# Kernel optimization log

Measured on AMD Instinct MI355X. Metric: run time of the kernel, lower is better.

Reference implementation:

```python
import jax, jax.numpy as jnp
from jax import lax
import numpy as np

# ---- constants mirroring args ----
T = 8192          # signal length
NUM_CH = 64       # eeg channels
LSTM_SIZE = 256
NUM_CLS = 40
NUM_PROP = 1024   # candidate proposals before NMS
NUM_PROP_AFTER = 256
PROP_LEN = 128    # extracted window length
IOU_THRESH = 0.5


def setup_inputs() -> dict:
    key = jax.random.key(0)
    ks = jax.random.split(key, 12)
    data = jax.random.normal(ks[0], (T, NUM_CH), dtype=jnp.float32)
    # proposals: (start, end, score), 1-D temporal intervals
    starts = jax.random.uniform(ks[1], (NUM_PROP,), minval=0.0, maxval=float(T - PROP_LEN))
    lens = jax.random.uniform(ks[2], (NUM_PROP,), minval=32.0, maxval=float(PROP_LEN))
    scores = jax.random.uniform(ks[3], (NUM_PROP,))
    proposals = jnp.stack([starts, starts + lens, scores], axis=-1).astype(jnp.float32)

    H, C = LSTM_SIZE, NUM_CH
    s_ih = 1.0 / np.sqrt(C)
    s_hh = 1.0 / np.sqrt(H)
    W_ih = jax.random.uniform(ks[4], (4 * H, C), minval=-s_ih, maxval=s_ih)
    W_hh = jax.random.uniform(ks[5], (4 * H, H), minval=-s_hh, maxval=s_hh)
    b_ih = jax.random.uniform(ks[6], (4 * H,), minval=-s_hh, maxval=s_hh)
    b_hh = jax.random.uniform(ks[7], (4 * H,), minval=-s_hh, maxval=s_hh)
    s_h = 1.0 / np.sqrt(H)
    W_cls = jax.random.uniform(ks[8], (NUM_CLS, H), minval=-s_h, maxval=s_h)
    b_cls = jax.random.uniform(ks[9], (NUM_CLS,), minval=-s_h, maxval=s_h)
    W_bbox = jax.random.uniform(ks[10], (2 * NUM_CLS, H), minval=-s_h, maxval=s_h)
    b_bbox = jax.random.uniform(ks[11], (2 * NUM_CLS,), minval=-s_h, maxval=s_h)
    return {"data": data, "proposals": proposals, "W_ih": W_ih, "W_hh": W_hh,
            "b_ih": b_ih, "b_hh": b_hh, "W_cls": W_cls, "b_cls": b_cls,
            "W_bbox": W_bbox, "b_bbox": b_bbox}


def _nms_1d(starts, ends, scores, iou_thresh):
    """Greedy 1-D interval NMS. Returns indices (into original order) of the
    first NUM_PROP_AFTER surviving proposals, in descending-score order."""
    order = jnp.argsort(-scores)
    s, e = starts[order], ends[order]
    n = s.shape[0]
    idx = jnp.arange(n)

    def body(i, sup):
        inter = jnp.maximum(0.0, jnp.minimum(e[i], e) - jnp.maximum(s[i], s))
        union = (e[i] - s[i]) + (e - s) - inter
        iou = inter / jnp.maximum(union, 1e-6)
        new = sup | ((iou > iou_thresh) & (idx > i) & (~sup[i]))
        return new

    suppressed = lax.fori_loop(0, n, body, jnp.zeros(n, dtype=bool))
    keep = ~suppressed
    # stable sort: kept proposals first, preserving score order
    sel = jnp.argsort(jnp.where(keep, 0, 1), stable=True)[:NUM_PROP_AFTER]
    return order[sel]


def _lstm_last(x, W_ih, W_hh, b_ih, b_hh):
    """x: [K, L, C]; returns last hidden state [K, H] (torch gate order ifgo)."""
    K = x.shape[0]
    H = W_hh.shape[1]
    h0 = jnp.zeros((K, H), x.dtype)
    c0 = jnp.zeros((K, H), x.dtype)
    b = b_ih + b_hh

    def step(carry, xt):
        h, c = carry
        gates = xt @ W_ih.T + h @ W_hh.T + b  # [K, 4H]
        i, f, g, o = jnp.split(gates, 4, axis=-1)
        i = jax.nn.sigmoid(i)
        f = jax.nn.sigmoid(f)
        g = jnp.tanh(g)
        o = jax.nn.sigmoid(o)
        c = f * c + i * g
        h = o * jnp.tanh(c)
        return (h, c), None

    (h, _), _ = lax.scan(step, (h0, c0), jnp.swapaxes(x, 0, 1))
    return h


def reference(data, proposals, W_ih, W_hh, b_ih, b_hh, W_cls, b_cls, W_bbox, b_bbox):
    starts, ends, scores = proposals[:, 0], proposals[:, 1], proposals[:, 2]
    # NMS + truncate to num_prop_after (training branch of original)
    kept = _nms_1d(starts, ends, scores, IOU_THRESH)            # [K]
    # extract fixed-length eeg windows at proposal starts (gather)
    t0 = jnp.clip(jnp.round(starts[kept]).astype(jnp.int32), 0, T - PROP_LEN)
    win_idx = t0[:, None] + jnp.arange(PROP_LEN)[None, :]       # [K, L]
    eeg_proposals = data[win_idx]                               # [K, L, C]
    # region LSTM -> last timestep feature
    base_feat = _lstm_last(eeg_proposals, W_ih, W_hh, b_ih, b_hh)  # [K, H]
    cls_feat = base_feat @ W_cls.T + b_cls                      # [K, num_cls]
    bbox_feat = base_feat @ W_bbox.T + b_bbox                   # [K, 2*num_cls]
    return cls_feat, bbox_feat
```

## Files before the change

kernel.cpp:

```cpp
#include <hip/hip_runtime.h>
#include <math.h>

#define T_LEN 8192
#define NUM_CH 64
#define HID 256
#define NUM_CLS 40
#define NUM_PROP 1024
#define NUM_PROP_AFTER 256
#define PROP_LEN 128

#define MS 4
#define NGRP 64
#define NSL 4
#define KH 320
#define KSEGN 4
#define SEGH 80

typedef _Float16 h2_t __attribute__((ext_vector_type(2)));
union U32H2 { unsigned int u; h2_t h; };
union HU16 { _Float16 h; unsigned short u; };

#if defined(__has_builtin)
#if __has_builtin(__builtin_amdgcn_fdot2)
#define HAS_FDOT2 1
#endif
#endif

__device__ __forceinline__ float dot2f(unsigned int wa, unsigned int hb, float acc) {
    U32H2 a, b;
    a.u = wa;
    b.u = hb;
#ifdef HAS_FDOT2
    return __builtin_amdgcn_fdot2(a.h, b.h, acc, false);
#else
    return acc + (float)a.h[0] * (float)b.h[0] + (float)a.h[1] * (float)b.h[1];
#endif
}

__device__ __forceinline__ float dot8f(const uint4& w, const uint4& h, float acc) {
    acc = dot2f(w.x, h.x, acc);
    acc = dot2f(w.y, h.y, acc);
    acc = dot2f(w.z, h.z, acc);
    acc = dot2f(w.w, h.w, acc);
    return acc;
}

__device__ __forceinline__ float fsigmoid(float x) { return 1.0f / (1.0f + __expf(-x)); }
__device__ __forceinline__ float ftanh(float x) {
    float e = __expf(-2.0f * fabsf(x));
    float t = (1.0f - e) / (1.0f + e);
    return copysignf(t, x);
}

__device__ __forceinline__ unsigned int pack2(float a, float b) {
    HU16 ha, hb;
    ha.h = (_Float16)a;
    hb.h = (_Float16)b;
    return (unsigned int)ha.u | ((unsigned int)hb.u << 16);
}

__global__ __launch_bounds__(1024, 4) void fused_kernel(
    const float* __restrict__ data, const float* __restrict__ prop,
    const float* __restrict__ W_ih, const float* __restrict__ W_hh,
    const float* __restrict__ b_ih, const float* __restrict__ b_hh,
    const float* __restrict__ W_cls, const float* __restrict__ b_cls,
    const float* __restrict__ W_bbox, const float* __restrict__ b_bbox,
    float* __restrict__ out, unsigned int* __restrict__ t0s,
    unsigned int* __restrict__ Hx, unsigned int* __restrict__ cnt) {
    __shared__ __align__(16) _Float16 hx[MS][KH];
    __shared__ __align__(16) float pp[MS][KSEGN][256];

    const int tid = threadIdx.x;
    const int g = blockIdx.x & (NGRP - 1);
    const int s = blockIdx.x >> 6;
    const int kseg = tid >> 8;
    const int rl = tid & 255;

    if (blockIdx.x == 0) {
        float* sc_p = &pp[0][0][0];
        float* ss = &pp[1][0][0];
        float* se = &pp[2][0][0];
        unsigned char* sup = (unsigned char*)&pp[3][0][0];
        unsigned long long* cmask =
            (unsigned long long*)((char*)&pp[3][0][0] + 1024);

        float ps = prop[tid * 3 + 0];
        float pe = prop[tid * 3 + 1];
        float pc = prop[tid * 3 + 2];
        sc_p[tid] = pc;
        sup[tid] = 0;
        __syncthreads();

        int r = 0;
        for (int j = 0; j < NUM_PROP; ++j) {
            float o = sc_p[j];
            r += (o > pc) || (o == pc && j < tid);
        }
        ss[r] = ps;
        se[r] = pe;
        __syncthreads();

        const float my_s = ss[tid];
        const float my_e = se[tid];
        const float my_len = my_e - my_s;
        bool mysup = false;

        for (int ci = 0; ci < 16; ++ci) {
            if (tid < 64) {
                int i = ci * 64 + tid;
                float is_ = ss[i], ie_ = se[i];
                unsigned long long m = __ballot(sup[i] != 0);
                for (int l = 0; l < 64; ++l) {
                    if (!((m >> l) & 1)) {
                        float ls = __shfl(is_, l);
                        float le = __shfl(ie_, l);
                        float inter = fmaxf(fminf(le, ie_) - fmaxf(ls, is_), 0.0f);
                        float uni = (le - ls) + (ie_ - is_) - inter;
                        float iou = inter / fmaxf(uni, 1e-6f);
                        unsigned long long nb = __ballot((tid > l) && (iou > 0.5f));
                        m |= nb;
                    }
                }
                sup[i] = (unsigned char)((m >> tid) & 1);
                if (tid == 0) cmask[ci] = ~m;
            }
            __syncthreads();
            unsigned long long am = cmask[ci];
            for (int l = 0; l < 64; ++l) {
                if ((am >> l) & 1) {
                    int i = ci * 64 + l;
                    if (tid > i && !mysup) {
                        float ls = ss[i], le = se[i];
                        float inter = fmaxf(fminf(le, my_e) - fmaxf(ls, my_s), 0.0f);
                        float uni = (le - ls) + my_len - inter;
                        if (inter / fmaxf(uni, 1e-6f) > 0.5f) mysup = true;
                    }
                }
            }
            sup[tid] = mysup ? 1 : 0;
            __syncthreads();
        }

        int myc = tid >> 6;
        unsigned long long mybit = 1ull << (tid & 63);
        int kb = 0, kt = 0;
        for (int c2 = 0; c2 < 16; ++c2) {
            int p = __popcll(cmask[c2]);
            kt += p;
            if (c2 < myc) kb += p;
        }
        kb += __popcll(cmask[myc] & (mybit - 1));
        int slot = (cmask[myc] & mybit) ? kb : (kt + (tid - kb));
        if (slot < NUM_PROP_AFTER) {
            int t0v = (int)rintf(my_s);
            t0v = max(0, min(t0v, T_LEN - PROP_LEN));
            __hip_atomic_store(&t0s[slot], (unsigned int)t0v | 0x80000000u,
                               __ATOMIC_RELAXED, __HIP_MEMORY_SCOPE_AGENT);
        }
        asm volatile("s_waitcnt vmcnt(0)" ::: "memory");
        __syncthreads();
    }

    uint4 Wr[10];
    {
        const int gate = rl >> 6, unit = rl & 63;
        const int grow = gate * 256 + s * 64 + unit;
        const float* __restrict__ baseh = W_hh + grow * HID;
        const float* __restrict__ basex = W_ih + grow * NUM_CH;
#pragma unroll
        for (int j = 0; j < 10; ++j) {
            const int kh = kseg * SEGH + j * 8;
            const float* src = (kh < 256) ? (baseh + kh) : (basex + (kh - 256));
            float4 f0 = *(const float4*)(src);
            float4 f1 = *(const float4*)(src + 4);
            Wr[j] = make_uint4(pack2(f0.x, f0.y), pack2(f0.z, f0.w),
                               pack2(f1.x, f1.y), pack2(f1.z, f1.w));
        }
    }

    const int aq = tid >> 6;
    const int au = tid & 63;
    float bi = 0.f, bf = 0.f, bg = 0.f, bo = 0.f, c_st = 0.f;
    if (tid < 256) {
        int u = s * 64 + au;
        bi = b_ih[u] + b_hh[u];
        bf = b_ih[256 + u] + b_hh[256 + u];
        bg = b_ih[512 + u] + b_hh[512 + u];
        bo = b_ih[768 + u] + b_hh[768 + u];
    }

    hx[tid >> 8][tid & 255] = (_Float16)0.0f;

    const int xs = (tid >> 6) & 3;
    const int xch = tid & 63;
    int xt0 = 0;
    if (tid >= 512 && tid < 768) {
        const unsigned int* tp = &t0s[g * MS + xs];
        unsigned int tv;
        for (;;) {
            tv = __hip_atomic_load(tp, __ATOMIC_RELAXED, __HIP_MEMORY_SCOPE_AGENT);
            if (tv & 0x80000000u) break;
            __builtin_amdgcn_s_sleep(8);
        }
        xt0 = (int)(tv & 0x7FFFFFFFu);
        hx[xs][256 + xch] = (_Float16)data[xt0 * NUM_CH + xch];
    }

    unsigned short* HxH = (unsigned short*)Hx;
    unsigned int* cg = &cnt[g * 16];
    __syncthreads();

    for (int t = 0; t < PROP_LEN; ++t) {
        float a0 = 0.f, a1 = 0.f, a2 = 0.f, a3 = 0.f;
#pragma unroll
        for (int j = 0; j < 10; ++j) {
            const int hb = kseg * SEGH + j * 8;
            uint4 h0 = *(const uint4*)&hx[0][hb];
            uint4 h1 = *(const uint4*)&hx[1][hb];
            uint4 h2 = *(const uint4*)&hx[2][hb];
            uint4 h3 = *(const uint4*)&hx[3][hb];
            uint4 w = Wr[j];
            a0 = dot8f(w, h0, a0);
            a1 = dot8f(w, h1, a1);
            a2 = dot8f(w, h2, a2);
            a3 = dot8f(w, h3, a3);
        }
        pp[0][kseg][rl] = a0;
        pp[1][kseg][rl] = a1;
        pp[2][kseg][rl] = a2;
        pp[3][kseg][rl] = a3;
        __syncthreads();

        if (tid < 256) {
            float si = pp[aq][0][au] + pp[aq][1][au] + pp[aq][2][au] +
                       pp[aq][3][au] + bi;
            float sf = pp[aq][0][64 + au] + pp[aq][1][64 + au] +
                       pp[aq][2][64 + au] + pp[aq][3][64 + au] + bf;
            float sg = pp[aq][0][128 + au] + pp[aq][1][128 + au] +
                       pp[aq][2][128 + au] + pp[aq][3][128 + au] + bg;
            float so = pp[aq][0][192 + au] + pp[aq][1][192 + au] +
                       pp[aq][2][192 + au] + pp[aq][3][192 + au] + bo;
            float gi = fsigmoid(si), gf = fsigmoid(sf);
            float gg = ftanh(sg), go = fsigmoid(so);
            c_st = gf * c_st + gi * gg;
            float h = go * ftanh(c_st);
            HU16 hu;
            hu.h = (_Float16)h;
            __hip_atomic_store(
                &HxH[((((t + 1) & 1) * NGRP + g) * MS + aq) * 256 + s * 64 + au],
                hu.u, __ATOMIC_RELAXED, __HIP_MEMORY_SCOPE_AGENT);
            asm volatile("s_waitcnt vmcnt(0)" ::: "memory");
            if (au == 0)
                __hip_atomic_fetch_add(cg, 1u, __ATOMIC_RELAXED,
                                       __HIP_MEMORY_SCOPE_AGENT);
        } else if (tid < 768 && t + 1 < PROP_LEN) {
            hx[xs][256 + xch] = (_Float16)data[(xt0 + t + 1) * NUM_CH + xch];
        }

        const unsigned int tgt = 16u * (unsigned int)(t + 1);
        if (tid == 0) {
            while (__hip_atomic_load(cg, __ATOMIC_RELAXED,
                                     __HIP_MEMORY_SCOPE_AGENT) < tgt) {
                __builtin_amdgcn_s_sleep(1);
            }
        }
        __syncthreads();
        if (tid < 512) {
            int sq = tid >> 7, w = tid & 127;
            unsigned int v = __hip_atomic_load(
                &Hx[((((t + 1) & 1) * NGRP + g) * MS + sq) * 128 + w],
                __ATOMIC_RELAXED, __HIP_MEMORY_SCOPE_AGENT);
            ((unsigned int*)hx)[sq * 160 + w] = v;
        }
        __syncthreads();
    }

    if (tid < MS * 30) {
        int sq = tid / 30;
        int ml = tid % 30;
        int m = s * 30 + ml;
        const float* Wrow;
        float acc;
        int oidx;
        if (m < NUM_CLS) {
            Wrow = W_cls + m * HID;
            acc = b_cls[m];
            oidx = (g * MS + sq) * NUM_CLS + m;
        } else {
            int mb = m - NUM_CLS;
            Wrow = W_bbox + mb * HID;
            acc = b_bbox[mb];
            oidx = NUM_PROP_AFTER * NUM_CLS + (g * MS + sq) * 2 * NUM_CLS + mb;
        }
        const float4* w4 = (const float4*)Wrow;
        const _Float16* hp = &hx[sq][0];
        for (int c = 0; c < 32; ++c) {
            float4 wa = w4[c * 2 + 0];
            float4 wb = w4[c * 2 + 1];
            acc += (float)hp[c * 8 + 0] * wa.x + (float)hp[c * 8 + 1] * wa.y +
                   (float)hp[c * 8 + 2] * wa.z + (float)hp[c * 8 + 3] * wa.w +
                   (float)hp[c * 8 + 4] * wb.x + (float)hp[c * 8 + 5] * wb.y +
                   (float)hp[c * 8 + 6] * wb.z + (float)hp[c * 8 + 7] * wb.w;
        }
        out[oidx] = acc;
    }
}

extern "C" void kernel_launch(void* const* d_in, const int* in_sizes, int n_in,
                              void* d_out, int out_size, void* d_ws,
                              size_t ws_size, hipStream_t stream) {
    const float* data = (const float*)d_in[0];
    const float* prop = (const float*)d_in[1];
    const float* W_ih = (const float*)d_in[2];
    const float* W_hh = (const float*)d_in[3];
    const float* b_ih = (const float*)d_in[4];
    const float* b_hh = (const float*)d_in[5];
    const float* W_cls = (const float*)d_in[6];
    const float* b_cls = (const float*)d_in[7];
    const float* W_bbox = (const float*)d_in[8];
    const float* b_bbox = (const float*)d_in[9];
    float* out = (float*)d_out;

    unsigned int* t0s = (unsigned int*)d_ws;
    unsigned int* cnt = (unsigned int*)((char*)d_ws + 1024);
    unsigned int* Hx = (unsigned int*)((char*)d_ws + 5120);

    hipMemsetAsync(d_ws, 0, 5120, stream);

    void* kargs[] = {(void*)&data,  (void*)&prop,   (void*)&W_ih,  (void*)&W_hh,
                     (void*)&b_ih,  (void*)&b_hh,   (void*)&W_cls, (void*)&b_cls,
                     (void*)&W_bbox, (void*)&b_bbox, (void*)&out,  (void*)&t0s,
                     (void*)&Hx,    (void*)&cnt};
    hipLaunchCooperativeKernel((void*)fused_kernel, dim3(NSL * NGRP), dim3(1024),
                               kargs, 0, stream);
}
```

Baseline: 746.3 us.

## Replace counter barrier with per-element tagged flags for cross-block hidden exchange

```diff
diff --git a/kernel.cpp b/kernel.cpp
--- a/kernel.cpp
+++ b/kernel.cpp
@@ -15,6 +15,7 @@
 #define KH 320
 #define KSEGN 4
 #define SEGH 80
+#define HXPAR 65536
 
 typedef _Float16 h2_t __attribute__((ext_vector_type(2)));
 union U32H2 { unsigned int u; h2_t h; };
@@ -66,7 +67,7 @@
     const float* __restrict__ W_cls, const float* __restrict__ b_cls,
     const float* __restrict__ W_bbox, const float* __restrict__ b_bbox,
     float* __restrict__ out, unsigned int* __restrict__ t0s,
-    unsigned int* __restrict__ Hx, unsigned int* __restrict__ cnt) {
+    unsigned int* __restrict__ Hx32) {
     __shared__ __align__(16) _Float16 hx[MS][KH];
     __shared__ __align__(16) float pp[MS][KSEGN][256];
 
@@ -181,6 +182,7 @@
     const int aq = tid >> 6;
     const int au = tid & 63;
     float bi = 0.f, bf = 0.f, bg = 0.f, bo = 0.f, c_st = 0.f;
+    int xt0 = 0;
     if (tid < 256) {
         int u = s * 64 + au;
         bi = b_ih[u] + b_hh[u];
@@ -189,13 +191,17 @@
         bo = b_ih[768 + u] + b_hh[768 + u];
     }
 
+    const int tid2 = tid - 256;
+    const int gp = tid2 >> 8;
+    const int gr = tid2 & 255;
+    const int gsq = gr >> 6, gu = gr & 63;
+    const int sp = gp + (gp >= s ? 1 : 0);
+    const unsigned int* gaddr = Hx32 + (g * MS + gsq) * HID + sp * 64 + gu;
+
     hx[tid >> 8][tid & 255] = (_Float16)0.0f;
 
-    const int xs = (tid >> 6) & 3;
-    const int xch = tid & 63;
-    int xt0 = 0;
-    if (tid >= 512 && tid < 768) {
-        const unsigned int* tp = &t0s[g * MS + xs];
+    if (tid < 256) {
+        const unsigned int* tp = &t0s[g * MS + aq];
         unsigned int tv;
         for (;;) {
             tv = __hip_atomic_load(tp, __ATOMIC_RELAXED, __HIP_MEMORY_SCOPE_AGENT);
@@ -203,14 +209,15 @@
             __builtin_amdgcn_s_sleep(8);
         }
         xt0 = (int)(tv & 0x7FFFFFFFu);
-        hx[xs][256 + xch] = (_Float16)data[xt0 * NUM_CH + xch];
-    }
-
-    unsigned short* HxH = (unsigned short*)Hx;
-    unsigned int* cg = &cnt[g * 16];
+        hx[aq][256 + au] = (_Float16)data[xt0 * NUM_CH + au];
+    }
     __syncthreads();
 
     for (int t = 0; t < PROP_LEN; ++t) {
+        float xnext = 0.0f;
+        if (tid < 256 && t + 1 < PROP_LEN)
+            xnext = data[(xt0 + t + 1) * NUM_CH + au];
+
         float a0 = 0.f, a1 = 0.f, a2 = 0.f, a3 = 0.f;
 #pragma unroll
         for (int j = 0; j < 10; ++j) {
@@ -231,6 +238,8 @@
         pp[3][kseg][rl] = a3;
         __syncthreads();
 
+        const unsigned int tagv = (unsigned int)(t + 1);
+        const int par = (t + 1) & 1;
         if (tid < 256) {
             float si = pp[aq][0][au] + pp[aq][1][au] + pp[aq][2][au] +
                        pp[aq][3][au] + bi;
@@ -247,30 +256,23 @@
             HU16 hu;
             hu.h = (_Float16)h;
             __hip_atomic_store(
-                &HxH[((((t + 1) & 1) * NGRP + g) * MS + aq) * 256 + s * 64 + au],
-                hu.u, __ATOMIC_RELAXED, __HIP_MEMORY_SCOPE_AGENT);
-            asm volatile("s_waitcnt vmcnt(0)" ::: "memory");
-            if (au == 0)
-                __hip_atomic_fetch_add(cg, 1u, __ATOMIC_RELAXED,
-                                       __HIP_MEMORY_SCOPE_AGENT);
-        } else if (tid < 768 && t + 1 < PROP_LEN) {
-            hx[xs][256 + xch] = (_Float16)data[(xt0 + t + 1) * NUM_CH + xch];
-        }
-
-        const unsigned int tgt = 16u * (unsigned int)(t + 1);
-        if (tid == 0) {
-            while (__hip_atomic_load(cg, __ATOMIC_RELAXED,
-                                     __HIP_MEMORY_SCOPE_AGENT) < tgt) {
+                &Hx32[par * HXPAR + (g * MS + aq) * HID + s * 64 + au],
+                (tagv << 16) | (unsigned int)hu.u, __ATOMIC_RELAXED,
+                __HIP_MEMORY_SCOPE_AGENT);
+            hx[aq][s * 64 + au] = hu.h;
+            if (t + 1 < PROP_LEN) hx[aq][256 + au] = (_Float16)xnext;
+        } else {
+            const unsigned int* ga = gaddr + par * HXPAR;
+            unsigned int v =
+                __hip_atomic_load(ga, __ATOMIC_RELAXED, __HIP_MEMORY_SCOPE_AGENT);
+            while (__builtin_expect((v >> 16) != tagv, 0)) {
                 __builtin_amdgcn_s_sleep(1);
+                v = __hip_atomic_load(ga, __ATOMIC_RELAXED,
+                                      __HIP_MEMORY_SCOPE_AGENT);
             }
-        }
-        __syncthreads();
-        if (tid < 512) {
-            int sq = tid >> 7, w = tid & 127;
-            unsigned int v = __hip_atomic_load(
-                &Hx[((((t + 1) & 1) * NGRP + g) * MS + sq) * 128 + w],
-                __ATOMIC_RELAXED, __HIP_MEMORY_SCOPE_AGENT);
-            ((unsigned int*)hx)[sq * 160 + w] = v;
+            HU16 hv;
+            hv.u = (unsigned short)(v & 0xFFFFu);
+            hx[gsq][sp * 64 + gu] = hv.h;
         }
         __syncthreads();
     }
@@ -322,15 +324,14 @@
     float* out = (float*)d_out;
 
     unsigned int* t0s = (unsigned int*)d_ws;
-    unsigned int* cnt = (unsigned int*)((char*)d_ws + 1024);
-    unsigned int* Hx = (unsigned int*)((char*)d_ws + 5120);
-
-    hipMemsetAsync(d_ws, 0, 5120, stream);
+    unsigned int* Hx32 = (unsigned int*)((char*)d_ws + 4096);
+
+    hipMemsetAsync(d_ws, 0, 4096 + 2 * HXPAR * 4, stream);
 
     void* kargs[] = {(void*)&data,  (void*)&prop,   (void*)&W_ih,  (void*)&W_hh,
                      (void*)&b_ih,  (void*)&b_hh,   (void*)&W_cls, (void*)&b_cls,
                      (void*)&W_bbox, (void*)&b_bbox, (void*)&out,  (void*)&t0s,
-                     (void*)&Hx,    (void*)&cnt};
+                     (void*)&Hx32};
     hipLaunchCooperativeKernel((void*)fused_kernel, dim3(NSL * NGRP), dim3(1024),
                                kargs, 0, stream);
 }
```

Measured after the change: 635.7 us. -14.8%, faster.
